# Kernel optimization log

Hardware: AMD Instinct MI355X
Metric: run time of the kernel (lower is better)

Reference implementation:

```python
import jax, jax.numpy as jnp
import numpy as np

B, H, W, IMG_CH = 64, 16, 16, 1024
N, TEXT_CH = 256, 768
FQ = FK = 512


def _glorot(key, shape, fan_in, fan_out):
    lim = np.sqrt(6.0 / (fan_in + fan_out)).astype(np.float32)
    return jax.random.uniform(key, shape, jnp.float32, -lim, lim)


def setup_inputs() -> dict:
    key = jax.random.key(0)
    ks = jax.random.split(key, 8)
    x1 = jax.random.normal(ks[0], (B, H, W, IMG_CH), jnp.float32)
    x2 = jax.random.normal(ks[1], (B, N, TEXT_CH), jnp.float32)
    # padding mask over text tokens, broadcast over image pixels
    masks = (jax.random.uniform(ks[2], (B, N, 1)) > 0.1).astype(jnp.float32)
    kernel_q = _glorot(ks[3], (1, 1, IMG_CH, FQ), IMG_CH, FQ)
    kernel_k = _glorot(ks[4], (1, TEXT_CH, FK), TEXT_CH, FK)
    kernel_v = _glorot(ks[5], (1, TEXT_CH, IMG_CH), TEXT_CH, IMG_CH)
    kernel_o = _glorot(ks[6], (1, 1, IMG_CH, IMG_CH), IMG_CH, IMG_CH)
    return {
        "x1": x1, "x2": x2, "masks": masks,
        "kernel_q": kernel_q, "bias_q": jnp.zeros((FQ,), jnp.float32),
        "kernel_k": kernel_k, "bias_k": jnp.zeros((FK,), jnp.float32),
        "kernel_v": kernel_v, "bias_v": jnp.zeros((IMG_CH,), jnp.float32),
        "kernel_o": kernel_o, "bias_o": jnp.zeros((IMG_CH,), jnp.float32),
    }


def reference(x1, x2, masks, kernel_q, bias_q, kernel_k, bias_k,
              kernel_v, bias_v, kernel_o, bias_o):
    b, h, w, c = x1.shape
    # 1x1 conv2d == pointwise matmul over channels
    q = jnp.einsum('bhwc,cf->bhwf', x1, kernel_q[0, 0]) + bias_q   # (B,H,W,512)
    # width-1 conv1d == pointwise matmul over channels
    k = jnp.einsum('bnc,cf->bnf', x2, kernel_k[0]) + bias_k        # (B,N,512)
    v = jnp.einsum('bnc,cf->bnf', x2, kernel_v[0]) + bias_v        # (B,N,IMG_CH)
    qf = q.reshape(b, h * w, -1)                                   # (B,HW,512)
    s = jnp.einsum('bqd,bnd->bqn', qf, k)                          # (B,HW,N)
    beta = jax.nn.softmax(s, axis=-1)
    # NON-STANDARD: mask applied AFTER softmax (no renormalization)
    beta = beta * jnp.swapaxes(masks, 1, 2)                        # (B,HW,N)*(B,1,N)
    o = jnp.einsum('bqn,bnf->bqf', beta, v).reshape(b, h, w, c)    # (B,H,W,IMG_CH)
    o = jnp.einsum('bhwc,cf->bhwf', o, kernel_o[0, 0]) + bias_o
    return o, beta
```

## Files before the change

### kernel.cpp

```cpp
#include <hip/hip_runtime.h>
#include <hip/hip_bf16.h>

using bf16 = __hip_bfloat16;

typedef __attribute__((ext_vector_type(8))) short short8;
typedef __attribute__((ext_vector_type(4))) short shortx4;
typedef __attribute__((ext_vector_type(4))) float f32x4;

#define MFMA_BF16(a, b, c) __builtin_amdgcn_mfma_f32_16x16x32_bf16((a), (b), (c), 0, 0, 0)

__device__ __forceinline__ void lds_load16(const void* g, void* l) {
    __builtin_amdgcn_global_load_lds(
        (const __attribute__((address_space(1))) void*)g,
        (__attribute__((address_space(3))) void*)l, 16, 0, 0);
}

__device__ __forceinline__ void swiz_xcd(int& bx, int& by) {
    const int NX = gridDim.x, NY = gridDim.y;
    const int flat = blockIdx.y * NX + blockIdx.x;
    const int cid = flat & 7, slot = flat >> 3;
    by = cid * (NY >> 3) + slot / NX;
    bx = slot % NX;
}

__device__ __forceinline__ void stage_bf16_128(const bf16* src, int ld, bf16* tile,
                                               int wave, int lane) {
    const int r = lane >> 2;
    const int c = ((lane & 3) ^ ((r >> 1) & 3)) * 8;
#pragma unroll
    for (int p = 0; p < 2; ++p) {
        const int row = p * 64 + wave * 16;
        lds_load16(src + (size_t)(row + r) * ld + c, tile + row * 32);
    }
}
__device__ __forceinline__ void stage_bf16_256_w8(const bf16* src, int ld, bf16* tile,
                                                  int wave, int lane) {
    const int r = lane >> 2;
    const int c = ((lane & 3) ^ ((r >> 1) & 3)) * 8;
#pragma unroll
    for (int p = 0; p < 2; ++p) {
        const int row = p * 128 + wave * 16;
        lds_load16(src + (size_t)(row + r) * ld + c, tile + row * 32);
    }
}
__device__ __forceinline__ void stage_f32_128(const float* src, int ld, float* tile,
                                              int wave, int lane) {
    const int r = lane >> 3;
    const int c = ((lane & 7) ^ r) * 4;
#pragma unroll
    for (int it = 0; it < 4; ++it) {
        const int row = it * 32 + wave * 8;
        lds_load16(src + (size_t)(row + r) * ld + c, tile + row * 32);
    }
}

__device__ __forceinline__ short8 rd_bf16(const bf16* tile, int row, int quad) {
    const int c = (quad ^ ((row >> 1) & 3)) * 8;
    return *(const short8*)(tile + row * 32 + c);
}
template <bool SPLIT>
__device__ __forceinline__ void rd_f32_hilo(const float* tile, int row, int quad,
                                            short8& h, short8& l) {
    const int f = row & 7;
    const f32x4 x0 = *(const f32x4*)(tile + row * 32 + ((2 * quad) ^ f) * 4);
    const f32x4 x1 = *(const f32x4*)(tile + row * 32 + ((2 * quad + 1) ^ f) * 4);
    float xs[8] = {x0[0], x0[1], x0[2], x0[3], x1[0], x1[1], x1[2], x1[3]};
#pragma unroll
    for (int j = 0; j < 8; ++j) {
        const bf16 hb = __float2bfloat16(xs[j]);
        h[j] = *(const short*)&hb;
        if constexpr (SPLIT) {
            const bf16 lb = __float2bfloat16(xs[j] - __bfloat162float(hb));
            l[j] = *(const short*)&lb;
        }
    }
}

template <bool SPLIT>
__global__ void transpose_split(const float* __restrict__ in, bf16* __restrict__ outh,
                                bf16* __restrict__ outl, int K, int N) {
    __shared__ float t[32][33];
    const int n0 = blockIdx.x * 32, k0 = blockIdx.y * 32;
    const int tx = threadIdx.x, ty = threadIdx.y;
#pragma unroll
    for (int i = 0; i < 4; ++i)
        t[ty + i * 8][tx] = in[(size_t)(k0 + ty + i * 8) * N + n0 + tx];
    __syncthreads();
#pragma unroll
    for (int i = 0; i < 4; ++i) {
        const float x = t[tx][ty + i * 8];
        const bf16 hb = __float2bfloat16(x);
        const size_t idx = (size_t)(n0 + ty + i * 8) * K + k0 + tx;
        outh[idx] = hb;
        if constexpr (SPLIT) outl[idx] = __float2bfloat16(x - __bfloat162float(hb));
    }
}

enum { G_SPLIT3 = 0, G_VT = 1, G_F32 = 2, G_PV = 3 };

template <int MODE>
__global__ __launch_bounds__(256) void gemm2(
    const void* __restrict__ Av, const bf16* __restrict__ Bth,
    const bf16* __restrict__ Btl, const float* __restrict__ bias,
    void* __restrict__ out0, void* __restrict__ out1, int N, int K) {
    constexpr bool ASPLIT = (MODE == G_SPLIT3);
    constexpr bool ACONV = (MODE == G_SPLIT3 || MODE == G_VT);
    constexpr int SZ_A = ACONV ? 128 * 32 * 4 : 128 * 32 * 2;
    constexpr int SZ_B = 128 * 32 * 2;
    constexpr int STAGE = SZ_A + SZ_B + (ASPLIT ? SZ_B : 0);
    constexpr int DBUF = 2 * STAGE;
    constexpr int SMEM =
        (MODE == G_VT) ? (DBUF > 128 * 136 * 2 ? DBUF : 128 * 136 * 2) : DBUF;
    __shared__ __align__(16) char smem[SMEM];
    bf16* Ts = (bf16*)smem;

    const int tid = threadIdx.x, wave = tid >> 6, lane = tid & 63;
    const int quad = lane >> 4, l15 = lane & 15;
    const int wr = wave >> 1, wc = wave & 1;

    int bx, by;
    if constexpr (MODE == G_PV) {
        bx = blockIdx.x;
        by = blockIdx.y;
    } else {
        swiz_xcd(bx, by);
    }
    const int m0 = by * 128, n0 = bx * 128;
    const int z = blockIdx.z;

    const float* Af = (const float*)Av;
    const bf16* Ab = (const bf16*)Av;
    const bf16* Bh = Bth;
    if constexpr (MODE == G_PV) {
        Ab += (size_t)z * 256 * 256;
        Bh += (size_t)z * 1024 * 256;
    }

    auto do_stage = [&](int k0, char* base) {
        if constexpr (ACONV)
            stage_f32_128(Af + (size_t)m0 * K + k0, K, (float*)base, wave, lane);
        else
            stage_bf16_128(Ab + (size_t)m0 * K + k0, K, (bf16*)base, wave, lane);
        stage_bf16_128(Bh + (size_t)n0 * K + k0, K, (bf16*)(base + SZ_A), wave, lane);
        if constexpr (ASPLIT)
            stage_bf16_128(Btl + (size_t)n0 * K + k0, K, (bf16*)(base + SZ_A + SZ_B),
                           wave, lane);
    };

    f32x4 acc[4][4] = {};
    const int nt = K / 32;
    do_stage(0, smem);
    __syncthreads();
    int cur = 0;
    for (int t = 0; t < nt; ++t) {
        char* base = smem + cur * STAGE;
        if (t + 1 < nt) do_stage((t + 1) * 32, smem + (cur ^ 1) * STAGE);

        const float* AsF = (const float*)base;
        const bf16* AsH = (const bf16*)base;
        const bf16* BsH = (const bf16*)(base + SZ_A);
        const bf16* BsL = (const bf16*)(base + SZ_A + SZ_B);

        short8 ah[4], al[4], bh[4], bl[4];
#pragma unroll
        for (int tt = 0; tt < 4; ++tt) {
            const int ra = wr * 64 + tt * 16 + l15;
            const int rb = wc * 64 + tt * 16 + l15;
            if constexpr (ACONV)
                rd_f32_hilo<ASPLIT>(AsF, ra, quad, ah[tt], al[tt]);
            else
                ah[tt] = rd_bf16(AsH, ra, quad);
            bh[tt] = rd_bf16(BsH, rb, quad);
            if constexpr (ASPLIT) bl[tt] = rd_bf16(BsL, rb, quad);
        }
        if constexpr (ASPLIT) {
#pragma unroll
            for (int ti = 0; ti < 4; ++ti)
#pragma unroll
                for (int tj = 0; tj < 4; ++tj) {
                    acc[ti][tj] = MFMA_BF16(al[ti], bh[tj], acc[ti][tj]);
                    acc[ti][tj] = MFMA_BF16(ah[ti], bl[tj], acc[ti][tj]);
                    acc[ti][tj] = MFMA_BF16(ah[ti], bh[tj], acc[ti][tj]);
                }
        } else {
#pragma unroll
            for (int ti = 0; ti < 4; ++ti)
#pragma unroll
                for (int tj = 0; tj < 4; ++tj)
                    acc[ti][tj] = MFMA_BF16(ah[ti], bh[tj], acc[ti][tj]);
        }
        __syncthreads();
        cur ^= 1;
    }

    float bv4[4] = {0.f, 0.f, 0.f, 0.f};
    if constexpr (MODE != G_PV) {
#pragma unroll
        for (int tj = 0; tj < 4; ++tj) bv4[tj] = bias[n0 + wc * 64 + tj * 16 + l15];
    }

    if constexpr (MODE == G_VT) {
#pragma unroll
        for (int ti = 0; ti < 4; ++ti)
#pragma unroll
            for (int tj = 0; tj < 4; ++tj)
#pragma unroll
                for (int i = 0; i < 4; ++i) {
                    const int ml = wr * 64 + ti * 16 + quad * 4 + i;
                    const int nl = wc * 64 + tj * 16 + l15;
                    Ts[nl * 136 + ml] = __float2bfloat16(acc[ti][tj][i] + bv4[tj]);
                }
        __syncthreads();
        const int bIdx = m0 >> 8, tok0 = m0 & 255;
        const int nl = tid >> 1, half = tid & 1;
        bf16* dst = (bf16*)out0 + ((size_t)bIdx * N + n0 + nl) * 256 + tok0 + half * 64;
        const bf16* src = &Ts[nl * 136 + half * 64];
#pragma unroll
        for (int j = 0; j < 8; ++j)
            *(short8*)(dst + j * 8) = *(const short8*)(src + j * 8);
    } else {
#pragma unroll
        for (int ti = 0; ti < 4; ++ti)
#pragma unroll
            for (int tj = 0; tj < 4; ++tj)
#pragma unroll
                for (int i = 0; i < 4; ++i) {
                    const size_t row = m0 + wr * 64 + ti * 16 + quad * 4 + i;
                    const size_t col = n0 + wc * 64 + tj * 16 + l15;
                    const float v = acc[ti][tj][i] + bv4[tj];
                    if constexpr (MODE == G_F32) {
                        ((float*)out0)[row * N + col] = v;
                    } else if constexpr (MODE == G_PV) {
                        ((bf16*)out0)[((size_t)z * 256 + row) * N + col] =
                            __float2bfloat16(v);
                    } else {
                        const bf16 hb = __float2bfloat16(v);
                        ((bf16*)out0)[row * N + col] = hb;
                        ((bf16*)out1)[row * N + col] =
                            __float2bfloat16(v - __bfloat162float(hb));
                    }
                }
    }
}

__global__ __launch_bounds__(512) void attn_s(
    const bf16* __restrict__ qh, const bf16* __restrict__ ql,
    const bf16* __restrict__ kh, const bf16* __restrict__ kl,
    const float* __restrict__ masks, float* __restrict__ beta_out,
    bf16* __restrict__ betaB) {
    __shared__ bf16 kH[2][256 * 32], kL[2][256 * 32];
    __shared__ float redM[4][32], redS[4][32];
    int qt, b;
    swiz_xcd(qt, b);
    const int tid = threadIdx.x, wave = tid >> 6, lane = tid & 63;
    const int quad = lane >> 4, l15 = lane & 15;
    const int wr = wave >> 2, wq = wave & 3;

    f32x4 acc[4] = {};
    const size_t qoff = ((size_t)(b * 256 + qt * 32 + wr * 16 + l15)) * 512;
    const size_t kbase = (size_t)(b * 256) * 512;

    stage_bf16_256_w8(kh + kbase, 512, kH[0], wave, lane);
    stage_bf16_256_w8(kl + kbase, 512, kL[0], wave, lane);
    __syncthreads();
    int cur = 0;
    for (int k0 = 0; k0 < 512; k0 += 32) {
        if (k0 + 32 < 512) {
            stage_bf16_256_w8(kh + kbase + k0 + 32, 512, kH[cur ^ 1], wave, lane);
            stage_bf16_256_w8(kl + kbase + k0 + 32, 512, kL[cur ^ 1], wave, lane);
        }
        const short8 aH = *(const short8*)(qh + qoff + k0 + quad * 8);
        const short8 aL = *(const short8*)(ql + qoff + k0 + quad * 8);
#pragma unroll
        for (int nt = 0; nt < 4; ++nt) {
            const int kr = wq * 64 + nt * 16 + l15;
            const short8 bH = rd_bf16(kH[cur], kr, quad);
            const short8 bL = rd_bf16(kL[cur], kr, quad);
            acc[nt] = MFMA_BF16(aH, bH, acc[nt]);
            acc[nt] = MFMA_BF16(aH, bL, acc[nt]);
            acc[nt] = MFMA_BF16(aL, bH, acc[nt]);
        }
        __syncthreads();
        cur ^= 1;
    }

    float pm[4], ps[4];
#pragma unroll
    for (int i = 0; i < 4; ++i) {
        float m = fmaxf(fmaxf(acc[0][i], acc[1][i]), fmaxf(acc[2][i], acc[3][i]));
#pragma unroll
        for (int s = 1; s < 16; s <<= 1) m = fmaxf(m, __shfl_xor(m, s));
        float sum = 0.f;
#pragma unroll
        for (int nt = 0; nt < 4; ++nt) sum += __expf(acc[nt][i] - m);
#pragma unroll
        for (int s = 1; s < 16; s <<= 1) sum += __shfl_xor(sum, s);
        pm[i] = m;
        ps[i] = sum;
    }
    if (l15 == 0) {
#pragma unroll
        for (int i = 0; i < 4; ++i) {
            redM[wq][wr * 16 + quad * 4 + i] = pm[i];
            redS[wq][wr * 16 + quad * 4 + i] = ps[i];
        }
    }
    __syncthreads();
    float gm[4], ginv[4];
#pragma unroll
    for (int i = 0; i < 4; ++i) {
        const int r = wr * 16 + quad * 4 + i;
        const float m = fmaxf(fmaxf(redM[0][r], redM[1][r]), fmaxf(redM[2][r], redM[3][r]));
        const float s = redS[0][r] * __expf(redM[0][r] - m) +
                        redS[1][r] * __expf(redM[1][r] - m) +
                        redS[2][r] * __expf(redM[2][r] - m) +
                        redS[3][r] * __expf(redM[3][r] - m);
        gm[i] = m;
        ginv[i] = 1.0f / s;
    }
#pragma unroll
    for (int nt = 0; nt < 4; ++nt) {
        const int col = wq * 64 + nt * 16 + l15;
        const float mv = masks[b * 256 + col];
#pragma unroll
        for (int i = 0; i < 4; ++i) {
            const int row = qt * 32 + wr * 16 + quad * 4 + i;
            const float bvv = __expf(acc[nt][i] - gm[i]) * ginv[i] * mv;
            const size_t idx = ((size_t)(b * 256 + row)) * 256 + col;
            beta_out[idx] = bvv;
            betaB[idx] = __float2bfloat16(bvv);
        }
    }
}

extern "C" void kernel_launch(void* const* d_in, const int* in_sizes, int n_in,
                              void* d_out, int out_size, void* d_ws, size_t ws_size,
                              hipStream_t stream) {
    const float* x1 = (const float*)d_in[0];
    const float* x2 = (const float*)d_in[1];
    const float* masks = (const float*)d_in[2];
    const float* Wq = (const float*)d_in[3];
    const float* bq = (const float*)d_in[4];
    const float* Wk = (const float*)d_in[5];
    const float* bk = (const float*)d_in[6];
    const float* Wv = (const float*)d_in[7];
    const float* bv = (const float*)d_in[8];
    const float* Wo = (const float*)d_in[9];
    const float* bo = (const float*)d_in[10];

    char* ws = (char*)d_ws;
    bf16* WqTh = (bf16*)(ws + 0);
    bf16* WqTl = (bf16*)(ws + 1048576);
    bf16* WkTh = (bf16*)(ws + 2097152);
    bf16* WkTl = (bf16*)(ws + 2883584);
    bf16* WvTh = (bf16*)(ws + 3670016);
    bf16* WoTh = (bf16*)(ws + 5242880);
    bf16* qh = (bf16*)(ws + 7340032);
    bf16* ql = (bf16*)(ws + 24117248);
    bf16* kh = (bf16*)(ws + 40894464);
    bf16* kl = (bf16*)(ws + 57671680);
    bf16* vT = (bf16*)(ws + 74448896);
    bf16* betaB = (bf16*)(ws + 108003328);
    bf16* o_mid = (bf16*)(ws + 7340032);

    float* out_o = (float*)d_out;
    float* out_beta = out_o + (size_t)16384 * 1024;

    const dim3 tb(32, 8);
    transpose_split<true><<<dim3(16, 32), tb, 0, stream>>>(Wq, WqTh, WqTl, 1024, 512);
    transpose_split<true><<<dim3(16, 24), tb, 0, stream>>>(Wk, WkTh, WkTl, 768, 512);
    transpose_split<false><<<dim3(32, 24), tb, 0, stream>>>(Wv, WvTh, nullptr, 768, 1024);
    transpose_split<false><<<dim3(32, 32), tb, 0, stream>>>(Wo, WoTh, nullptr, 1024, 1024);

    gemm2<G_SPLIT3><<<dim3(4, 128), 256, 0, stream>>>(x1, WqTh, WqTl, bq, qh, ql, 512, 1024);
    gemm2<G_SPLIT3><<<dim3(4, 128), 256, 0, stream>>>(x2, WkTh, WkTl, bk, kh, kl, 512, 768);
    gemm2<G_VT><<<dim3(8, 128), 256, 0, stream>>>(x2, WvTh, nullptr, bv, vT, nullptr, 1024, 768);

    attn_s<<<dim3(8, 64), 512, 0, stream>>>(qh, ql, kh, kl, masks, out_beta, betaB);

    gemm2<G_PV><<<dim3(8, 2, 64), 256, 0, stream>>>(betaB, vT, nullptr, nullptr, o_mid,
                                                    nullptr, 1024, 256);
    gemm2<G_F32><<<dim3(8, 128), 256, 0, stream>>>(o_mid, WoTh, nullptr, bo, out_o,
                                                   nullptr, 1024, 1024);
}
```

Before: 416.9 us.

## Prefetch two stages ahead with vmcnt waits instead of full syncthreads

The GEMM and score kernels now issue loads two K-steps ahead into the double buffer. Each iteration waits with a partial s_waitcnt vmcnt, so only the current stage's global-to-LDS loads must finish, rather than a full __syncthreads drain. Fragments are read into registers, then a barrier lets the next prefetch overwrite the buffer just consumed before the MFMAs run. This aims to overlap global load latency with compute. It relies on hand-counted per-thread load counts (SLOADS, 4) matching the staging helpers, and a wrong count risks a race.

```diff
diff --git a/kernel.cpp b/kernel.cpp
--- a/kernel.cpp
+++ b/kernel.cpp
@@ -4,7 +4,6 @@
 using bf16 = __hip_bfloat16;
 
 typedef __attribute__((ext_vector_type(8))) short short8;
-typedef __attribute__((ext_vector_type(4))) short shortx4;
 typedef __attribute__((ext_vector_type(4))) float f32x4;
 
 #define MFMA_BF16(a, b, c) __builtin_amdgcn_mfma_f32_16x16x32_bf16((a), (b), (c), 0, 0, 0)
@@ -13,6 +12,14 @@
     __builtin_amdgcn_global_load_lds(
         (const __attribute__((address_space(1))) void*)g,
         (__attribute__((address_space(3))) void*)l, 16, 0, 0);
+}
+
+template <int N>
+__device__ __forceinline__ void waitvm() {
+    asm volatile("s_waitcnt vmcnt(%0)" ::"n"(N) : "memory");
+}
+__device__ __forceinline__ void lgkm0_fence() {
+    asm volatile("s_waitcnt lgkmcnt(0)" ::: "memory");
 }
 
 __device__ __forceinline__ void swiz_xcd(int& bx, int& by) {
@@ -111,6 +118,7 @@
     constexpr int DBUF = 2 * STAGE;
     constexpr int SMEM =
         (MODE == G_VT) ? (DBUF > 128 * 136 * 2 ? DBUF : 128 * 136 * 2) : DBUF;
+    constexpr int SLOADS = ACONV ? (ASPLIT ? 8 : 6) : 4;
     __shared__ __align__(16) char smem[SMEM];
     bf16* Ts = (bf16*)smem;
 
@@ -150,12 +158,16 @@
     f32x4 acc[4][4] = {};
     const int nt = K / 32;
     do_stage(0, smem);
-    __syncthreads();
+    do_stage(32, smem + STAGE);
     int cur = 0;
     for (int t = 0; t < nt; ++t) {
+        if (t + 1 < nt)
+            waitvm<SLOADS>();
+        else
+            waitvm<0>();
+        __builtin_amdgcn_s_barrier();
+
         char* base = smem + cur * STAGE;
-        if (t + 1 < nt) do_stage((t + 1) * 32, smem + (cur ^ 1) * STAGE);
-
         const float* AsF = (const float*)base;
         const bf16* AsH = (const bf16*)base;
         const bf16* BsH = (const bf16*)(base + SZ_A);
@@ -173,6 +185,10 @@
             bh[tt] = rd_bf16(BsH, rb, quad);
             if constexpr (ASPLIT) bl[tt] = rd_bf16(BsL, rb, quad);
         }
+        lgkm0_fence();
+        __builtin_amdgcn_s_barrier();
+        if (t + 2 < nt) do_stage((t + 2) * 32, base);
+
         if constexpr (ASPLIT) {
 #pragma unroll
             for (int ti = 0; ti < 4; ++ti)
@@ -189,7 +205,6 @@
                 for (int tj = 0; tj < 4; ++tj)
                     acc[ti][tj] = MFMA_BF16(ah[ti], bh[tj], acc[ti][tj]);
         }
-        __syncthreads();
         cur ^= 1;
     }
 
@@ -262,25 +277,38 @@
 
     stage_bf16_256_w8(kh + kbase, 512, kH[0], wave, lane);
     stage_bf16_256_w8(kl + kbase, 512, kL[0], wave, lane);
-    __syncthreads();
+    stage_bf16_256_w8(kh + kbase + 32, 512, kH[1], wave, lane);
+    stage_bf16_256_w8(kl + kbase + 32, 512, kL[1], wave, lane);
     int cur = 0;
-    for (int k0 = 0; k0 < 512; k0 += 32) {
-        if (k0 + 32 < 512) {
-            stage_bf16_256_w8(kh + kbase + k0 + 32, 512, kH[cur ^ 1], wave, lane);
-            stage_bf16_256_w8(kl + kbase + k0 + 32, 512, kL[cur ^ 1], wave, lane);
-        }
+    for (int t = 0; t < 16; ++t) {
+        const int k0 = t * 32;
+        if (t + 1 < 16)
+            waitvm<4>();
+        else
+            waitvm<0>();
+        __builtin_amdgcn_s_barrier();
+
         const short8 aH = *(const short8*)(qh + qoff + k0 + quad * 8);
         const short8 aL = *(const short8*)(ql + qoff + k0 + quad * 8);
+        short8 bH[4], bL[4];
 #pragma unroll
         for (int nt = 0; nt < 4; ++nt) {
             const int kr = wq * 64 + nt * 16 + l15;
-            const short8 bH = rd_bf16(kH[cur], kr, quad);
-            const short8 bL = rd_bf16(kL[cur], kr, quad);
-            acc[nt] = MFMA_BF16(aH, bH, acc[nt]);
-            acc[nt] = MFMA_BF16(aH, bL, acc[nt]);
-            acc[nt] = MFMA_BF16(aL, bH, acc[nt]);
-        }
-        __syncthreads();
+            bH[nt] = rd_bf16(kH[cur], kr, quad);
+            bL[nt] = rd_bf16(kL[cur], kr, quad);
+        }
+        lgkm0_fence();
+        __builtin_amdgcn_s_barrier();
+        if (t + 2 < 16) {
+            stage_bf16_256_w8(kh + kbase + (t + 2) * 32, 512, kH[cur], wave, lane);
+            stage_bf16_256_w8(kl + kbase + (t + 2) * 32, 512, kL[cur], wave, lane);
+        }
+#pragma unroll
+        for (int nt = 0; nt < 4; ++nt) {
+            acc[nt] = MFMA_BF16(aH, bH[nt], acc[nt]);
+            acc[nt] = MFMA_BF16(aH, bL[nt], acc[nt]);
+            acc[nt] = MFMA_BF16(aL, bH[nt], acc[nt]);
+        }
         cur ^= 1;
     }
 
```

After: 413.6 us. Within noise of the previous version (-0.8%).
